# Kernel optimization log

Hardware: AMD Instinct MI355X
Metric: run time of the kernel (lower is better)

Reference implementation:

```python
import jax, jax.numpy as jnp
import numpy as np

B, S, H, DH = 8, 2048, 4, 32
D = H * DH  # all_head_size = true_hidden_size = 128


def setup_inputs() -> dict:
    key = jax.random.key(0)
    ks = jax.random.split(key, 9)
    inp = {
        "query_tensor": jax.random.normal(ks[0], (B, S, D), dtype=jnp.float32),
        "key_tensor": jax.random.normal(ks[1], (B, S, D), dtype=jnp.float32),
        "value_tensor": jax.random.normal(ks[2], (B, S, D), dtype=jnp.float32),
        "attention_mask": jnp.zeros((B, 1, 1, S), dtype=jnp.float32),
        "head_mask": jnp.ones((1, H, 1, 1), dtype=jnp.float32),
        "Wq": jax.random.normal(ks[3], (D, D), dtype=jnp.float32) * 0.02,
        "bq": jnp.zeros((D,), dtype=jnp.float32),
        "Wk": jax.random.normal(ks[4], (D, D), dtype=jnp.float32) * 0.02,
        "bk": jnp.zeros((D,), dtype=jnp.float32),
        "Wv": jax.random.normal(ks[5], (D, D), dtype=jnp.float32) * 0.02,
        "bv": jnp.zeros((D,), dtype=jnp.float32),
    }
    return inp


def _split_heads(x):
    # (B, S, D) -> (B, H, S, DH)
    return x.reshape(B, S, H, DH).transpose(0, 2, 1, 3)


def reference(query_tensor, key_tensor, value_tensor, attention_mask, head_mask,
              Wq, bq, Wk, bk, Wv, bv):
    q = _split_heads(query_tensor @ Wq + bq)   # (B,H,S,DH)
    k = _split_heads(key_tensor @ Wk + bk)
    v = _split_heads(value_tensor @ Wv + bv)

    scale = 1.0 / jnp.sqrt(jnp.float32(DH))
    scores = jnp.einsum("bhqd,bhkd->bhqk", q, k) * scale + attention_mask
    probs = jax.nn.softmax(scores, axis=-1)
    # dropout is identity at inference (training=False)
    probs = probs * head_mask
    ctx = jnp.einsum("bhqk,bhkd->bhqd", probs, v)  # (B,H,S,DH)
    ctx = ctx.transpose(0, 2, 1, 3).reshape(B, S, D)
    return ctx
```

## Files before the change

kernel.cpp:

```cpp
#include <hip/hip_runtime.h>
#include <hip/hip_bf16.h>
#include <math.h>

#define B_ 8
#define S_ 2048
#define H_ 4
#define DH_ 32
#define D_ 128
#define BS_ (B_ * S_)
#define LOG2E 1.4426950408889634f
#define QSCALE (0.17677669529663687f * LOG2E)

typedef float f32x4  __attribute__((ext_vector_type(4)));
typedef float f32x16 __attribute__((ext_vector_type(16)));
typedef short s16x8  __attribute__((ext_vector_type(8)));

__device__ __forceinline__ unsigned short bf(float x) {
    return __builtin_bit_cast(unsigned short, __float2bfloat16(x));
}
__device__ __forceinline__ float bf2f(unsigned short u) {
    return __builtin_bit_cast(float, (unsigned int)u << 16);
}
__device__ __forceinline__ unsigned int pk2(float a, float b) {
    unsigned int r;
    asm("v_cvt_pk_bf16_f32 %0, %1, %2" : "=v"(r) : "v"(a), "v"(b));
    return r;
}
__device__ __forceinline__ void pswap(unsigned int& a, unsigned int& b) {
    asm volatile("v_permlane32_swap_b32 %0, %1" : "+v"(a), "+v"(b));
}
__device__ __forceinline__ void gll16(const void* g, void* l) {
    __builtin_amdgcn_global_load_lds(
        (const __attribute__((address_space(1))) unsigned int*)(g),
        (__attribute__((address_space(3))) unsigned int*)(l), 16, 0, 0);
}

#define OFF_Q  0u
#define OFF_K  2097152u
#define OFF_V  4194304u
#define OFF_W  6291456u
#define OFF_E  6389760u

__global__ __launch_bounds__(256) void wprep(
    const float* __restrict__ Wq, const float* __restrict__ Wk, const float* __restrict__ Wv,
    const float* __restrict__ maskg,
    unsigned short* __restrict__ Wt, unsigned short* __restrict__ Em)
{
    if (blockIdx.z == 3) {
        const int id16 = blockIdx.y * 4 + blockIdx.x;
        const int base = id16 * 1024 + threadIdx.x * 4;
        float4 m4 = *(const float4*)&maskg[base];
        ushort4 o;
        o.x = bf(__builtin_amdgcn_exp2f(m4.x * LOG2E));
        o.y = bf(__builtin_amdgcn_exp2f(m4.y * LOG2E));
        o.z = bf(__builtin_amdgcn_exp2f(m4.z * LOG2E));
        o.w = bf(__builtin_amdgcn_exp2f(m4.w * LOG2E));
        *(ushort4*)&Em[base] = o;
        return;
    }
    const float* W = (blockIdx.z == 0) ? Wq : (blockIdx.z == 1) ? Wk : Wv;
    unsigned short* Oh = Wt + (size_t)blockIdx.z * D_ * D_;
    unsigned short* Ol = Oh + 3 * D_ * D_;
    __shared__ float tf[32][36];
    const int t = threadIdx.x;
    const int kt = blockIdx.x * 32, ct = blockIdx.y * 32;
    {
        int kl = t >> 3, cl = (t & 7) * 4;
        float4 w4 = *(const float4*)&W[(size_t)(kt + kl) * D_ + ct + cl];
        tf[kl][cl + 0] = w4.x; tf[kl][cl + 1] = w4.y;
        tf[kl][cl + 2] = w4.z; tf[kl][cl + 3] = w4.w;
    }
    __syncthreads();
    {
        int cl = t >> 3, kl = (t & 7) * 4;
        ushort4 oh, ol;
        float v;
        v = tf[kl + 0][cl]; oh.x = bf(v); ol.x = bf(v - bf2f(oh.x));
        v = tf[kl + 1][cl]; oh.y = bf(v); ol.y = bf(v - bf2f(oh.y));
        v = tf[kl + 2][cl]; oh.z = bf(v); ol.z = bf(v - bf2f(oh.z));
        v = tf[kl + 3][cl]; oh.w = bf(v); ol.w = bf(v - bf2f(oh.w));
        *(ushort4*)&Oh[(size_t)(ct + cl) * D_ + kt + kl] = oh;
        *(ushort4*)&Ol[(size_t)(ct + cl) * D_ + kt + kl] = ol;
    }
}

__global__ __launch_bounds__(256) void qkv_mfma(
    const float* __restrict__ Xq, const float* __restrict__ Xk, const float* __restrict__ Xv,
    const unsigned short* __restrict__ Wt, const float* __restrict__ maskg,
    const float* __restrict__ bq, const float* __restrict__ bk, const float* __restrict__ bv,
    unsigned short* __restrict__ Qo, unsigned short* __restrict__ Kf,
    unsigned short* __restrict__ Vf)
{
    const int mode = blockIdx.z, chalf = blockIdx.y;
    const float* X; const float* bias; float scl;
    if (mode == 0)      { X = Xq; bias = bq; scl = QSCALE; }
    else if (mode == 1) { X = Xk; bias = bk; scl = 1.f; }
    else                { X = Xv; bias = bv; scl = 1.f; }
    const unsigned short* WmH = Wt + (size_t)mode * D_ * D_;
    const unsigned short* WmL = WmH + 3 * D_ * D_;

    __shared__ __align__(16) unsigned short xa[2 * 32 * 136];
    __shared__ __align__(16) unsigned short wt[2 * 64 * 136];

    const int t = threadIdx.x;
    const long row0 = (long)blockIdx.x * 32;

    #pragma unroll
    for (int j = 0; j < 8; j++) {
        int idx = t + 256 * j;
        int part = idx >> 10, i2 = idx & 1023;
        int r = i2 >> 4, c16 = i2 & 15;
        const unsigned short* src = part ? WmL : WmH;
        uint4 v = *(const uint4*)&src[(size_t)(chalf * 64 + r) * D_ + c16 * 8];
        *(uint4*)&wt[part * 8704 + r * 136 + c16 * 8] = v;
    }
    #pragma unroll
    for (int j = 0; j < 4; j++) {
        int idx = t + 256 * j;
        int r = idx >> 5, c4 = idx & 31;
        float4 v = *(const float4*)(X + (row0 + r) * D_ + c4 * 4);
        ushort4 ph, pl;
        ph.x = bf(v.x); pl.x = bf(v.x - bf2f(ph.x));
        ph.y = bf(v.y); pl.y = bf(v.y - bf2f(ph.y));
        ph.z = bf(v.z); pl.z = bf(v.z - bf2f(ph.z));
        ph.w = bf(v.w); pl.w = bf(v.w - bf2f(ph.w));
        *(ushort4*)&xa[r * 136 + c4 * 4] = ph;
        *(ushort4*)&xa[4352 + r * 136 + c4 * 4] = pl;
    }
    __syncthreads();

    const int w = t >> 6, lane = t & 63, lo = lane & 15, hi = lane >> 4;
    const int mf = w >> 1, nb = (w & 1) * 2;
    f32x4 acc[2] = {};
    #pragma unroll
    for (int kk = 0; kk < 4; kk++) {
        const int ko = kk * 32 + hi * 8;
        s16x8 ah = *(const s16x8*)&xa[(mf * 16 + lo) * 136 + ko];
        s16x8 al = *(const s16x8*)&xa[4352 + (mf * 16 + lo) * 136 + ko];
        #pragma unroll
        for (int n2 = 0; n2 < 2; n2++) {
            const int nf = nb + n2;
            s16x8 bh2 = *(const s16x8*)&wt[(nf * 16 + lo) * 136 + ko];
            s16x8 bl2 = *(const s16x8*)&wt[8704 + (nf * 16 + lo) * 136 + ko];
            acc[n2] = __builtin_amdgcn_mfma_f32_16x16x32_bf16(ah, bh2, acc[n2], 0, 0, 0);
            acc[n2] = __builtin_amdgcn_mfma_f32_16x16x32_bf16(al, bh2, acc[n2], 0, 0, 0);
            acc[n2] = __builtin_amdgcn_mfma_f32_16x16x32_bf16(ah, bl2, acc[n2], 0, 0, 0);
        }
    }
    __syncthreads();

    const long b_i = row0 >> 11;
    const long s0g = row0 & 2047;

    if (mode < 2) {
        #pragma unroll
        for (int n2 = 0; n2 < 2; n2++) {
            int c_l = (nb + n2) * 16 + lo;
            float bb = bias[chalf * 64 + c_l];
            #pragma unroll
            for (int r = 0; r < 4; r++) {
                int s = mf * 16 + hi * 4 + r;
                xa[s * 72 + c_l] = bf((acc[n2][r] + bb) * scl);
            }
        }
        __syncthreads();
        int s = t >> 3, part = t & 7;
        int c_g = chalf * 64 + part * 8;
        int h = c_g >> 5, dd = c_g & 31;
        long s_i = s0g + s;
        int bh = (int)(b_i * H_ + h);
        uint4 val = *(const uint4*)&xa[s * 72 + part * 8];
        if (mode == 0) {
            *(uint4*)(Qo + ((size_t)bh * S_ + s_i) * DH_ + dd) = val;
        } else {
            int fr = dd >> 4, hwd = (dd >> 3) & 1;
            size_t off = ((((size_t)bh * 64 + (s_i >> 5)) * 2 + fr) * 64
                          + (s_i & 31) + hwd * 32) * 8;
            *(uint4*)(Kf + off) = val;
        }
    } else {
        float emr[4];
        #pragma unroll
        for (int r = 0; r < 4; r++) {
            const int s_l = mf * 16 + hi * 4 + r;
            emr[r] = __builtin_amdgcn_exp2f(maskg[b_i * S_ + s0g + s_l] * LOG2E);
        }
        #pragma unroll
        for (int n2 = 0; n2 < 2; n2++) {
            int c_l = (nb + n2) * 16 + lo;
            float bb = bias[chalf * 64 + c_l];
            #pragma unroll
            for (int r = 0; r < 4; r++) {
                int s = mf * 16 + hi * 4 + r;
                xa[c_l * 68 + s] = bf((acc[n2][r] + bb) * emr[r]);
            }
        }
        __syncthreads();
        if (t < 128) {
            int c_l = t >> 1, sh2 = (t & 1) * 16;
            int c_g = chalf * 64 + c_l;
            int h = c_g >> 5, dd = c_g & 31;
            long key0 = s0g + sh2;
            int bh = (int)(b_i * H_ + h);
            size_t base = (((size_t)bh * 128 + (key0 >> 4)) * 64 + dd) * 8;
            uint2 p0 = *(const uint2*)&xa[c_l * 68 + sh2 + 0];
            uint2 p1 = *(const uint2*)&xa[c_l * 68 + sh2 + 4];
            uint2 p2 = *(const uint2*)&xa[c_l * 68 + sh2 + 8];
            uint2 p3 = *(const uint2*)&xa[c_l * 68 + sh2 + 12];
            *(uint4*)(Vf + base)       = make_uint4(p0.x, p0.y, p1.x, p1.y);
            *(uint4*)(Vf + base + 256) = make_uint4(p2.x, p2.y, p3.x, p3.y);
        }
    }
}

__global__ __launch_bounds__(512, 2) void flash_mfma(
    const unsigned short* __restrict__ Qg, const unsigned short* __restrict__ Kfg,
    const unsigned short* __restrict__ Vfg, const unsigned short* __restrict__ Emg,
    const float* __restrict__ head_mask, float* __restrict__ Out)
{
    __shared__ __align__(16) unsigned short ksh[2][4096];
    __shared__ __align__(16) unsigned short vsh[2][4096];
    __shared__ float ms[2][2][64][33];

    const int t = threadIdx.x, w = t >> 6, lane = t & 63;
    const int l31 = lane & 31, hw = lane >> 5;
    const int kq = w & 3, qh = w >> 2;

    const int lid = blockIdx.x;
    const int xcd = lid & 7, ser = lid >> 3;
    const int bh = xcd * 4 + (ser >> 5);
    const int qi = ser & 31;
    const int b = bh >> 2, h = bh & 3;
    const int q0 = qi * 64 + qh * 32;

    const unsigned short* qp = Qg + ((size_t)bh * S_ + q0 + l31) * DH_ + hw * 8;
    const s16x8 qf0 = *(const s16x8*)qp;
    const s16x8 qf1 = *(const s16x8*)(qp + 16);

    const size_t kvbase = (size_t)bh * 65536;
    const unsigned short* ksrc = Kfg + kvbase + (size_t)w * 512 + (size_t)lane * 8;
    const unsigned short* vsrc = Vfg + kvbase + (size_t)w * 512 + (size_t)lane * 8;
    const unsigned short* ep   = Emg + (size_t)b * S_ + kq * 32 + hw * 8;

    gll16(ksrc, &ksh[0][w * 512]);
    gll16(vsrc, &vsh[0][w * 512]);
    s16x8 ef0 = *(const s16x8*)(ep);
    s16x8 ef1 = *(const s16x8*)(ep + 16);
    __syncthreads();

    f32x16 ctx = {}, lacc = {};
    const f32x16 z16 = {};

    for (int tile = 0; tile < 16; tile++) {
        const int cur = tile & 1, nxt = cur ^ 1;

        s16x8 en0, en1;
        if (tile < 15) {
            gll16(ksrc + (size_t)(tile + 1) * 4096, &ksh[nxt][w * 512]);
            gll16(vsrc + (size_t)(tile + 1) * 4096, &vsh[nxt][w * 512]);
            en0 = *(const s16x8*)(ep + (tile + 1) * 128);
            en1 = *(const s16x8*)(ep + (tile + 1) * 128 + 16);
        }

        const unsigned short* kb = &ksh[cur][kq * 1024];
        const unsigned short* vb = &vsh[cur][kq * 1024];
        const s16x8 kf0 = *(const s16x8*)(kb + (size_t)lane * 8);
        const s16x8 kf1 = *(const s16x8*)(kb + 512 + (size_t)lane * 8);
        const s16x8 vf0 = *(const s16x8*)(vb + (size_t)lane * 8);
        const s16x8 vf1 = *(const s16x8*)(vb + 512 + (size_t)lane * 8);

        __builtin_amdgcn_s_setprio(1);
        f32x16 s = __builtin_amdgcn_mfma_f32_32x32x16_bf16(kf0, qf0, z16, 0, 0, 0);
        s = __builtin_amdgcn_mfma_f32_32x32x16_bf16(kf1, qf1, s, 0, 0, 0);
        __builtin_amdgcn_s_setprio(0);

        unsigned int pd[8];
        #pragma unroll
        for (int j = 0; j < 8; j++) {
            const float p0 = __builtin_amdgcn_exp2f(s[2 * j]);
            const float p1 = __builtin_amdgcn_exp2f(s[2 * j + 1]);
            pd[j] = pk2(p0, p1);
        }
        pswap(pd[0], pd[2]); pswap(pd[1], pd[3]);
        pswap(pd[4], pd[6]); pswap(pd[5], pd[7]);
        const s16x8 pa0 = __builtin_bit_cast(s16x8, make_uint4(pd[0], pd[1], pd[2], pd[3]));
        const s16x8 pa1 = __builtin_bit_cast(s16x8, make_uint4(pd[4], pd[5], pd[6], pd[7]));

        __builtin_amdgcn_s_setprio(1);
        ctx  = __builtin_amdgcn_mfma_f32_32x32x16_bf16(pa0, vf0, ctx, 0, 0, 0);
        lacc = __builtin_amdgcn_mfma_f32_32x32x16_bf16(pa0, ef0, lacc, 0, 0, 0);
        ctx  = __builtin_amdgcn_mfma_f32_32x32x16_bf16(pa1, vf1, ctx, 0, 0, 0);
        lacc = __builtin_amdgcn_mfma_f32_32x32x16_bf16(pa1, ef1, lacc, 0, 0, 0);
        __builtin_amdgcn_s_setprio(0);

        __syncthreads();
        if (tile < 15) { ef0 = en0; ef1 = en1; }
    }

    if (kq >= 2) {
        float* d = &ms[qh][kq - 2][lane][0];
        #pragma unroll
        for (int r = 0; r < 16; r++) { d[r] = ctx[r]; d[16 + r] = lacc[r]; }
    }
    __syncthreads();
    if (kq < 2) {
        const float* sr = &ms[qh][kq][lane][0];
        #pragma unroll
        for (int r = 0; r < 16; r++) { ctx[r] += sr[r]; lacc[r] += sr[16 + r]; }
    }
    __syncthreads();
    if (kq == 1) {
        float* d = &ms[qh][0][lane][0];
        #pragma unroll
        for (int r = 0; r < 16; r++) { d[r] = ctx[r]; d[16 + r] = lacc[r]; }
    }
    __syncthreads();
    if (kq == 0) {
        const float* sr = &ms[qh][0][lane][0];
        #pragma unroll
        for (int r = 0; r < 16; r++) { ctx[r] += sr[r]; lacc[r] += sr[16 + r]; }
        const float hm = head_mask[h];
        #pragma unroll
        for (int r = 0; r < 16; r++) {
            const int qrow = (r & 3) + 8 * (r >> 2) + 4 * hw;
            Out[((size_t)b * S_ + q0 + qrow) * D_ + h * DH_ + l31] = ctx[r] * hm / lacc[r];
        }
    }
}

extern "C" void kernel_launch(void* const* d_in, const int* in_sizes, int n_in,
                              void* d_out, int out_size, void* d_ws, size_t ws_size,
                              hipStream_t stream) {
    const float* Xq   = (const float*)d_in[0];
    const float* Xk   = (const float*)d_in[1];
    const float* Xv   = (const float*)d_in[2];
    const float* mask = (const float*)d_in[3];
    const float* hm   = (const float*)d_in[4];
    const float* Wq   = (const float*)d_in[5];
    const float* bq   = (const float*)d_in[6];
    const float* Wk   = (const float*)d_in[7];
    const float* bk   = (const float*)d_in[8];
    const float* Wv   = (const float*)d_in[9];
    const float* bv   = (const float*)d_in[10];
    float* out = (float*)d_out;

    unsigned short* ws = (unsigned short*)d_ws;
    unsigned short* Qo = ws + OFF_Q;
    unsigned short* Kf = ws + OFF_K;
    unsigned short* Vf = ws + OFF_V;
    unsigned short* Wt = ws + OFF_W;
    unsigned short* Em = ws + OFF_E;

    wprep<<<dim3(4, 4, 4), 256, 0, stream>>>(Wq, Wk, Wv, mask, Wt, Em);
    qkv_mfma<<<dim3(BS_ / 32, 2, 3), 256, 0, stream>>>(Xq, Xk, Xv, Wt, mask,
                                                       bq, bk, bv, Qo, Kf, Vf);
    flash_mfma<<<dim3(1024), 512, 0, stream>>>(Qo, Kf, Vf, Em, hm, out);
}
```

Baseline: 61.02 us.

## Triple-buffer K/V tiles with explicit vmcnt waits and preload mask row into LDS

Replaces the double-buffered K/V staging with a three-slot ring that prefetches two tiles ahead. Each iteration waits with explicit s_waitcnt vmcnt and a single barrier instead of a trailing __syncthreads. The mask row for the batch is loaded once into shared memory rather than fetched from global each tile. The reduction scratch now aliases the K/V buffer region to keep LDS use down, and the occupancy hint is removed from launch bounds, which may change register allocation and occupancy.

```diff
diff --git a/kernel.cpp b/kernel.cpp
--- a/kernel.cpp
+++ b/kernel.cpp
@@ -213,14 +213,12 @@
     }
 }
 
-__global__ __launch_bounds__(512, 2) void flash_mfma(
+__global__ __launch_bounds__(512) void flash_mfma(
     const unsigned short* __restrict__ Qg, const unsigned short* __restrict__ Kfg,
     const unsigned short* __restrict__ Vfg, const unsigned short* __restrict__ Emg,
     const float* __restrict__ head_mask, float* __restrict__ Out)
 {
-    __shared__ __align__(16) unsigned short ksh[2][4096];
-    __shared__ __align__(16) unsigned short vsh[2][4096];
-    __shared__ float ms[2][2][64][33];
+    __shared__ __align__(16) unsigned short smem[26624];
 
     const int t = threadIdx.x, w = t >> 6, lane = t & 63;
     const int l31 = lane & 31, hw = lane >> 5;
@@ -237,37 +235,46 @@
     const s16x8 qf0 = *(const s16x8*)qp;
     const s16x8 qf1 = *(const s16x8*)(qp + 16);
 
+    *(uint2*)&smem[24576 + t * 4] = *(const uint2*)(Emg + (size_t)b * S_ + t * 4);
+
     const size_t kvbase = (size_t)bh * 65536;
     const unsigned short* ksrc = Kfg + kvbase + (size_t)w * 512 + (size_t)lane * 8;
     const unsigned short* vsrc = Vfg + kvbase + (size_t)w * 512 + (size_t)lane * 8;
-    const unsigned short* ep   = Emg + (size_t)b * S_ + kq * 32 + hw * 8;
-
-    gll16(ksrc, &ksh[0][w * 512]);
-    gll16(vsrc, &vsh[0][w * 512]);
-    s16x8 ef0 = *(const s16x8*)(ep);
-    s16x8 ef1 = *(const s16x8*)(ep + 16);
-    __syncthreads();
+
+    gll16(ksrc,        &smem[0 * 4096 + w * 512]);
+    gll16(vsrc,        &smem[12288 + 0 * 4096 + w * 512]);
+    gll16(ksrc + 4096, &smem[1 * 4096 + w * 512]);
+    gll16(vsrc + 4096, &smem[12288 + 1 * 4096 + w * 512]);
+
+    asm volatile("s_waitcnt lgkmcnt(0)" ::: "memory");
+    __builtin_amdgcn_sched_barrier(0);
 
     f32x16 ctx = {}, lacc = {};
     const f32x16 z16 = {};
 
     for (int tile = 0; tile < 16; tile++) {
-        const int cur = tile & 1, nxt = cur ^ 1;
-
-        s16x8 en0, en1;
-        if (tile < 15) {
-            gll16(ksrc + (size_t)(tile + 1) * 4096, &ksh[nxt][w * 512]);
-            gll16(vsrc + (size_t)(tile + 1) * 4096, &vsh[nxt][w * 512]);
-            en0 = *(const s16x8*)(ep + (tile + 1) * 128);
-            en1 = *(const s16x8*)(ep + (tile + 1) * 128 + 16);
-        }
-
-        const unsigned short* kb = &ksh[cur][kq * 1024];
-        const unsigned short* vb = &vsh[cur][kq * 1024];
+        const int cur = tile % 3;
+
+        if (tile < 15) { asm volatile("s_waitcnt vmcnt(2)" ::: "memory"); }
+        else           { asm volatile("s_waitcnt vmcnt(0)" ::: "memory"); }
+        __builtin_amdgcn_sched_barrier(0);
+        __builtin_amdgcn_s_barrier();
+        __builtin_amdgcn_sched_barrier(0);
+
+        if (tile < 14) {
+            const int pb = (tile + 2) % 3;
+            gll16(ksrc + (size_t)(tile + 2) * 4096, &smem[pb * 4096 + w * 512]);
+            gll16(vsrc + (size_t)(tile + 2) * 4096, &smem[12288 + pb * 4096 + w * 512]);
+        }
+
+        const unsigned short* kb = &smem[cur * 4096 + kq * 1024];
+        const unsigned short* vb = &smem[12288 + cur * 4096 + kq * 1024];
         const s16x8 kf0 = *(const s16x8*)(kb + (size_t)lane * 8);
         const s16x8 kf1 = *(const s16x8*)(kb + 512 + (size_t)lane * 8);
         const s16x8 vf0 = *(const s16x8*)(vb + (size_t)lane * 8);
         const s16x8 vf1 = *(const s16x8*)(vb + 512 + (size_t)lane * 8);
+        const s16x8 ef0 = *(const s16x8*)&smem[24576 + tile * 128 + kq * 32 + hw * 8];
+        const s16x8 ef1 = *(const s16x8*)&smem[24576 + tile * 128 + kq * 32 + hw * 8 + 16];
 
         __builtin_amdgcn_s_setprio(1);
         f32x16 s = __builtin_amdgcn_mfma_f32_32x32x16_bf16(kf0, qf0, z16, 0, 0, 0);
@@ -292,33 +299,42 @@
         ctx  = __builtin_amdgcn_mfma_f32_32x32x16_bf16(pa1, vf1, ctx, 0, 0, 0);
         lacc = __builtin_amdgcn_mfma_f32_32x32x16_bf16(pa1, ef1, lacc, 0, 0, 0);
         __builtin_amdgcn_s_setprio(0);
-
-        __syncthreads();
-        if (tile < 15) { ef0 = en0; ef1 = en1; }
-    }
+    }
+
+    __syncthreads();
+    float* ms = (float*)smem;
+    #define MS(qh_, sl_, ln_, r_) ms[(((qh_) * 2 + (sl_)) * 64 + (ln_)) * 33 + (r_)]
 
     if (kq >= 2) {
-        float* d = &ms[qh][kq - 2][lane][0];
-        #pragma unroll
-        for (int r = 0; r < 16; r++) { d[r] = ctx[r]; d[16 + r] = lacc[r]; }
+        #pragma unroll
+        for (int r = 0; r < 16; r++) {
+            MS(qh, kq - 2, lane, r) = ctx[r];
+            MS(qh, kq - 2, lane, 16 + r) = lacc[r];
+        }
     }
     __syncthreads();
     if (kq < 2) {
-        const float* sr = &ms[qh][kq][lane][0];
-        #pragma unroll
-        for (int r = 0; r < 16; r++) { ctx[r] += sr[r]; lacc[r] += sr[16 + r]; }
+        #pragma unroll
+        for (int r = 0; r < 16; r++) {
+            ctx[r]  += MS(qh, kq, lane, r);
+            lacc[r] += MS(qh, kq, lane, 16 + r);
+        }
     }
     __syncthreads();
     if (kq == 1) {
-        float* d = &ms[qh][0][lane][0];
-        #pragma unroll
-        for (int r = 0; r < 16; r++) { d[r] = ctx[r]; d[16 + r] = lacc[r]; }
+        #pragma unroll
+        for (int r = 0; r < 16; r++) {
+            MS(qh, 0, lane, r) = ctx[r];
+            MS(qh, 0, lane, 16 + r) = lacc[r];
+        }
     }
     __syncthreads();
     if (kq == 0) {
-        const float* sr = &ms[qh][0][lane][0];
-        #pragma unroll
-        for (int r = 0; r < 16; r++) { ctx[r] += sr[r]; lacc[r] += sr[16 + r]; }
+        #pragma unroll
+        for (int r = 0; r < 16; r++) {
+            ctx[r]  += MS(qh, 0, lane, r);
+            lacc[r] += MS(qh, 0, lane, 16 + r);
+        }
         const float hm = head_mask[h];
         #pragma unroll
         for (int r = 0; r < 16; r++) {
@@ -326,6 +342,7 @@
             Out[((size_t)b * S_ + q0 + qrow) * D_ + h * DH_ + l31] = ctx[r] * hm / lacc[r];
         }
     }
+    #undef MS
 }
 
 extern "C" void kernel_launch(void* const* d_in, const int* in_sizes, int n_in,
```

Measured after the change: 55.37 us. -9.3%, faster.
